# Optimization experiments

Measured on AMD Instinct MI355X. Metric: run time of the kernel, lower is better.

The kernel has to match this reference:

```python
import jax, jax.numpy as jnp
import numpy as np

KH, KW, PAD = 32, 32, 10  # kernel_size and padding from NeuralMem.__init__


def setup_inputs() -> dict:
    key = jax.random.key(0)
    k1, k2, k3, k4 = jax.random.split(key, 4)
    image = jax.random.normal(k1, (64, 64, 3), dtype=jnp.float32)
    mem = jax.random.normal(k2, (8192, 3072), dtype=jnp.float32)    # faiss IndexFlatL2 bank (keys)
    mem2 = jax.random.normal(k3, (8192, 3072), dtype=jnp.float32)   # faiss reconstruction bank (values)
    mapping = jax.random.randint(k4, (8192,), 0, 8192)              # Counter.most_common(1) vote table
    return {"image": image, "mem": mem, "mem2": mem2, "mapping": mapping}


def reference(image, mem, mem2, mapping):
    H, W, C = image.shape
    x = image.transpose(2, 0, 1)                       # [C,H,W]  (permute(2,0,1))
    xp = jnp.pad(x, ((0, 0), (PAD, PAD), (PAD, PAD)))  # unfold padding
    Lh = H + 2 * PAD - KH + 1
    Lw = W + 2 * PAD - KW + 1
    ii = jnp.arange(Lh)[:, None] + jnp.arange(KH)[None, :]  # [Lh,KH]
    jj = jnp.arange(Lw)[:, None] + jnp.arange(KW)[None, :]  # [Lw,KW]
    # unfold: patches [C,Lh,KH,Lw,KW] -> [L, C*KH*KW] with torch's (C,kh,kw) column order
    patches = xp[:, ii[:, :, None, None], jj[None, None, :, :]]
    patches = patches.transpose(1, 3, 0, 2, 4).reshape(Lh * Lw, C * KH * KW)  # [L,D]
    # L2 kNN (k=1): argmin ||p - m||^2 = argmin (||m||^2 - 2 p.m); ||p||^2 is constant per row
    mem_sq = jnp.sum(mem * mem, axis=1)                # [N]
    scores = patches @ mem.T                           # [L,N]
    nn = jnp.argmin(mem_sq[None, :] - 2.0 * scores, axis=1)  # [L]
    # counter majority vote -> mem2 reconstruct
    recon = mem2[mapping[nn]]                          # [L,D]
    # fold (sum of overlapping patches), then crop padding
    rp = recon.reshape(Lh, Lw, C, KH, KW).transpose(2, 0, 3, 1, 4)  # [C,Lh,KH,Lw,KW]
    outp = jnp.zeros_like(xp).at[:, ii[:, :, None, None], jj[None, None, :, :]].add(rp)
    out = outp[:, PAD:PAD + H, PAD:PAD + W]            # [C,H,W]
    out = out / jnp.max(out)                           # out / out.flatten().max()
    return out.transpose(1, 2, 0)                      # [H,W,C]
```

## Files before the change

kernel.cpp:

```cpp
#include <hip/hip_runtime.h>

typedef unsigned short u16;
typedef unsigned int   u32;
typedef unsigned long long u64;
typedef int      i32x4  __attribute__((ext_vector_type(4)));
typedef float    f32x4  __attribute__((ext_vector_type(4)));
typedef _Float16 f16x8  __attribute__((ext_vector_type(8)));

#define LHW   53
#define NP    2809
#define KDIM  3072
#define NMEM  8192
#define PADW  84
#define IMG   64
#define MPAD  2816
#define BIGF  3.402823466e+38f
#define MARGIN 24.0f
#define QS    31.75f
#define C2    (2.0f / (QS * QS))

#define O_XP    0UL
#define O_MSQ   84736UL
#define O_MI8   117504UL
#define O_AI8   25283328UL
#define O_D     33934080UL
#define O_PVAL  80071424UL
#define O_ROWI  81524480UL
#define O_ACC   81535744UL
#define WS_NEED5 81584896UL

#define F_XP    0
#define F_MSQ   21504
#define F_PVAL  29696
#define F_PIDX  119584
#define F_ROW   209472
#define F_ACC   212288
#define F_MAX   224576
#define NSPL    32
#define NRANGE  (NMEM / NSPL)

__device__ inline char q8(float x) {
    float y = x * QS;
    y = fminf(fmaxf(y, -127.f), 127.f);
    return (char)__float2int_rn(y);
}

__global__ void k_xp(const float* __restrict__ image, float* __restrict__ xp,
                     float* __restrict__ accb) {
    int id = blockIdx.x * 256 + threadIdx.x;
    if (id < 12288) accb[id] = 0.f;
    if (id < 3 * PADW * PADW) {
        int c = id / (PADW * PADW), rem = id % (PADW * PADW);
        int py = rem / PADW, px = rem % PADW;
        float v = 0.f;
        if (py >= 10 && py < 74 && px >= 10 && px < 74)
            v = image[((py - 10) * IMG + (px - 10)) * 3 + c];
        xp[id] = v;
    }
}

__global__ __launch_bounds__(1024) void k_maxnorm(const float* __restrict__ acc,
                                                  float* __restrict__ out) {
    int t = threadIdx.x;
    float m = -BIGF;
    for (int i = t; i < 12288; i += 1024) m = fmaxf(m, acc[i]);
    #pragma unroll
    for (int s = 1; s < 64; s <<= 1) m = fmaxf(m, __shfl_xor(m, s));
    __shared__ float ls[16];
    int lane = t & 63, w = t >> 6;
    if (lane == 0) ls[w] = m;
    __syncthreads();
    float mv = ls[0];
    #pragma unroll
    for (int i = 1; i < 16; ++i) mv = fmaxf(mv, ls[i]);
    for (int i = t; i < 12288; i += 1024) {
        int c = i >> 12, y = (i >> 6) & 63, x = i & 63;
        out[(y * IMG + x) * 3 + c] = acc[i] / mv;
    }
}

__global__ __launch_bounds__(256) void k_quantmsq(const float* __restrict__ mem,
                                                  char* __restrict__ mq,
                                                  float* __restrict__ msq) {
    int j = blockIdx.x, t = threadIdx.x;
    const float4* r4 = (const float4*)(mem + (size_t)j * KDIM);
    char4* q4 = (char4*)(mq + (size_t)j * KDIM);
    float s = 0.f;
    #pragma unroll
    for (int i = 0; i < 3; ++i) {
        int idx = i * 256 + t;
        float4 v = r4[idx];
        s += v.x * v.x + v.y * v.y + v.z * v.z + v.w * v.w;
        char4 q = {q8(v.x), q8(v.y), q8(v.z), q8(v.w)};
        q4[idx] = q;
    }
    #pragma unroll
    for (int m = 1; m < 64; m <<= 1) s += __shfl_xor(s, m);
    __shared__ float ls[4];
    int lane = t & 63, w = t >> 6;
    if (lane == 0) ls[w] = s;
    __syncthreads();
    if (t == 0) msq[j] = ls[0] + ls[1] + ls[2] + ls[3];
}

__global__ __launch_bounds__(256) void k_quant_A(const float* __restrict__ xp,
                                                 char* __restrict__ aq) {
    int id = blockIdx.x * 256 + threadIdx.x;
    int e0 = id * 4;
    int p = e0 / KDIM, k = e0 - p * KDIM;
    char4 q = {0, 0, 0, 0};
    if (p < NP) {
        int c = k >> 10, kh = (k >> 5) & 31, kw = k & 31;
        int lh = p / LHW, lw = p - lh * LHW;
        const float* src = xp + c * (PADW * PADW) + (lh + kh) * PADW + lw + kw;
        q.x = q8(src[0]); q.y = q8(src[1]); q.z = q8(src[2]); q.w = q8(src[3]);
    }
    ((char4*)aq)[id] = q;
}

__global__ __launch_bounds__(256) void k_gemm_i8(
    const char* __restrict__ Aq, const char* __restrict__ Bq,
    const float* __restrict__ msq, _Float16* __restrict__ Dm,
    float* __restrict__ pval)
{
    __shared__ __align__(16) char lds[65536];
    const int t = threadIdx.x;
    const int lane = t & 63;
    const int w = t >> 6, wm = w >> 1, wn = w & 1;
    const int mrow = lane & 15;

    int L = blockIdx.x;
    int logical = (L & 7) * 176 + (L >> 3);
    int by = logical / 22, bx = logical - by * 22;
    const int rowBase = bx * 128;
    const int jBase   = by * 128;

    const int lrow = lane >> 3;
    const int gsrc = (lane & 7) ^ lrow;
    const char* gpl[8];
    unsigned ldsb[8];
    #pragma unroll
    for (int s = 0; s < 8; ++s) {
        int P = s >> 2, sub = s & 3;
        int row = sub * 32 + w * 8 + lrow;
        const char* basep = (P == 0 ? Aq : Bq);
        int gRow = (P == 0 ? rowBase : jBase) + row;
        gpl[s]  = basep + (size_t)gRow * KDIM + gsrc * 16;
        ldsb[s] = P * 16384 + (unsigned)(sub * 32 + w * 8) * 128;
    }

    i32x4 acc[4][4];
    #pragma unroll
    for (int i = 0; i < 4; ++i)
        #pragma unroll
        for (int j = 0; j < 4; ++j) { i32x4 z = {0, 0, 0, 0}; acc[i][j] = z; }

    #pragma unroll
    for (int s = 0; s < 8; ++s)
        __builtin_amdgcn_global_load_lds(
            (const __attribute__((address_space(1))) void*)(gpl[s]),
            (__attribute__((address_space(3))) void*)(lds + ldsb[s]),
            16, 0, 0);

    for (int kc = 0; kc < 24; ++kc) {
        const int cb = kc & 1;
        __syncthreads();
        if (kc < 23) {
            const unsigned nb = (cb ^ 1) * 32768u;
            #pragma unroll
            for (int s = 0; s < 8; ++s)
                __builtin_amdgcn_global_load_lds(
                    (const __attribute__((address_space(1))) void*)(gpl[s] + (kc + 1) * 128),
                    (__attribute__((address_space(3))) void*)(lds + nb + ldsb[s]),
                    16, 0, 0);
        }
        const char* lbase = lds + cb * 32768;
        #pragma unroll
        for (int kh2 = 0; kh2 < 2; ++kh2) {
            const int grp = kh2 * 4 + (lane >> 4);
            i32x4 ah[4];
            #pragma unroll
            for (int f = 0; f < 4; ++f) {
                int ra = wm * 64 + f * 16 + mrow;
                ah[f] = *(const i32x4*)(lbase + ra * 128 + (grp ^ (ra & 7)) * 16);
            }
            #pragma unroll
            for (int fj = 0; fj < 4; ++fj) {
                int rb = wn * 64 + fj * 16 + mrow;
                i32x4 bh = *(const i32x4*)(lbase + 16384 + rb * 128 + (grp ^ (rb & 7)) * 16);
                #pragma unroll
                for (int fi = 0; fi < 4; ++fi)
                    acc[fi][fj] = __builtin_amdgcn_mfma_i32_16x16x64_i8(ah[fi], bh, acc[fi][fj], 0, 0, 0);
            }
        }
    }

    float ms[4];
    #pragma unroll
    for (int fj = 0; fj < 4; ++fj) ms[fj] = msq[jBase + wn * 64 + fj * 16 + mrow] - 3072.0f;
    const int splitId = by * 2 + wn;
    #pragma unroll
    for (int fi = 0; fi < 4; ++fi) {
        #pragma unroll
        for (int r = 0; r < 4; ++r) {
            int p = rowBase + wm * 64 + fi * 16 + (lane >> 4) * 4 + r;
            float bv = BIGF;
            #pragma unroll
            for (int fj = 0; fj < 4; ++fj) {
                int j = jBase + wn * 64 + fj * 16 + mrow;
                float d = fmaf(-C2, (float)acc[fi][fj][r], ms[fj]);
                Dm[(size_t)p * NMEM + j] = (_Float16)d;
                bv = fminf(bv, d);
            }
            #pragma unroll
            for (int m = 1; m < 16; m <<= 1) bv = fminf(bv, __shfl_xor(bv, m));
            if (mrow == 0 && p < NP)
                pval[(size_t)p * 128 + splitId] = bv;
        }
    }
}

__global__ __launch_bounds__(256) void k_refine(
    const _Float16* __restrict__ Dm, const float* __restrict__ pval,
    const float* __restrict__ msq, const float* __restrict__ xp,
    const float* __restrict__ mem, const int* __restrict__ mapping,
    int* __restrict__ rowIdx)
{
    const int p = blockIdx.x, t = threadIdx.x;
    const _Float16* row = Dm + (size_t)p * NMEM;
    const int lane = t & 63, w = t >> 6;

    __shared__ float wred[4];
    __shared__ int lcnt;
    __shared__ int list[256];
    __shared__ float thr_s;

    float pm = (t < 128) ? pval[(size_t)p * 128 + t] : BIGF;
    #pragma unroll
    for (int m = 1; m < 64; m <<= 1) pm = fminf(pm, __shfl_xor(pm, m));
    if (lane == 0) wred[w] = pm;
    if (t == 0) lcnt = 0;
    __syncthreads();
    if (t == 0)
        thr_s = fminf(fminf(wred[0], wred[1]), fminf(wred[2], wred[3]))
                + (MARGIN + 0.5f);
    __syncthreads();
    const float th = thr_s;

    #pragma unroll
    for (int i0 = 0; i0 < 4; ++i0) {
        int base = i0 * 2048 + t * 8;
        f16x8 v = *(const f16x8*)(row + base);
        #pragma unroll
        for (int e = 0; e < 8; ++e)
            if ((float)v[e] <= th) {
                int sl = atomicAdd(&lcnt, 1);
                if (sl < 256) list[sl] = base + e;
            }
    }
    __syncthreads();
    int nc = min(lcnt, 256);

    const int lh = p / LHW, lw = p - (p / LHW) * LHW;
    float bd = BIGF; int bj = 0x7fffffff;
    __shared__ float tot;
    for (int ci = 0; ci < nc; ++ci) {
        int j = list[ci];
        const float* mrow2 = mem + (size_t)j * KDIM;
        float s = 0.f;
        for (int k = t; k < KDIM; k += 256) {
            int c = k >> 10, kh = (k >> 5) & 31, kw = k & 31;
            s += xp[c * (PADW * PADW) + (lh + kh) * PADW + lw + kw] * mrow2[k];
        }
        #pragma unroll
        for (int m = 1; m < 64; m <<= 1) s += __shfl_xor(s, m);
        if (lane == 0) wred[w] = s;
        __syncthreads();
        if (t == 0) tot = wred[0] + wred[1] + wred[2] + wred[3];
        __syncthreads();
        float d = msq[j] - 2.f * tot;
        if (d < bd || (d == bd && j < bj)) { bd = d; bj = j; }
    }
    if (t == 0) rowIdx[p] = mapping[bj];
}

__global__ __launch_bounds__(256) void k_scatter(const float* __restrict__ mem2,
                                                 const int* __restrict__ rowIdx,
                                                 float* __restrict__ accb) {
    const int lh = blockIdx.x / 3, c = blockIdx.x % 3;
    __shared__ float accs[32 * 85];
    __shared__ int r2s[53];
    const int t = threadIdx.x;
    for (int i = t; i < 32 * 85; i += 256) accs[i] = 0.f;
    if (t < 53) r2s[t] = rowIdx[lh * LHW + t];
    __syncthreads();
    const int kh  = t >> 3;
    const int kwb = (t & 7) * 4;
    const size_t coff = (size_t)c * 1024 + kh * 32 + kwb;
    float* a0 = accs + kh * 85 + kwb;
    for (int lw = 0; lw < 53; ++lw) {
        const float4 v = *(const float4*)(mem2 + (size_t)r2s[lw] * KDIM + coff);
        float* a = a0 + lw;
        a[0] += v.x; a[1] += v.y; a[2] += v.z; a[3] += v.w;
        __syncthreads();
    }
    for (int i = t; i < 32 * 84; i += 256) {
        int kh2 = i / 84, px = i - kh2 * 84;
        int y = lh + kh2 - 10, x = px - 10;
        if (y >= 0 && y < 64 && x >= 0 && x < 64)
            atomicAdd(&accb[c * 4096 + y * 64 + x], accs[kh2 * 85 + px]);
    }
}

__global__ __launch_bounds__(256) void k_msq(const float* __restrict__ mem,
                                             float* __restrict__ msq) {
    int j = blockIdx.x;
    const float* row = mem + (size_t)j * KDIM;
    float s = 0.f;
    for (int i = threadIdx.x; i < KDIM; i += 256) { float v = row[i]; s += v * v; }
    #pragma unroll
    for (int m = 1; m < 64; m <<= 1) s += __shfl_xor(s, m);
    __shared__ float ls[4];
    int lane = threadIdx.x & 63, w = threadIdx.x >> 6;
    if (lane == 0) ls[w] = s;
    __syncthreads();
    if (threadIdx.x == 0) msq[j] = ls[0] + ls[1] + ls[2] + ls[3];
}

__global__ void k_amin(const float* __restrict__ pval, const int* __restrict__ pidx,
                       const int* __restrict__ mapping, int* __restrict__ rowIdx,
                       int nspl) {
    int p = blockIdx.x * 256 + threadIdx.x;
    if (p < NP) {
        float bv = BIGF; int bi = 0x7fffffff;
        for (int ns = 0; ns < nspl; ++ns) {
            float v = pval[(size_t)p * nspl + ns];
            int ix = pidx[(size_t)p * nspl + ns];
            if (v < bv || (v == bv && ix < bi)) { bv = v; bi = ix; }
        }
        rowIdx[p] = mapping[bi];
    }
}

__global__ __launch_bounds__(256) void k_gather(const float* __restrict__ mem2,
                                                const int* __restrict__ rowIdx,
                                                float* __restrict__ acc) {
    int b = blockIdx.x;
    int c = b >> 12, y = (b >> 6) & 63, x = b & 63;
    int khmin = max(0, y - 42), khmax = min(31, y + 10);
    int kwmin = max(0, x - 42), kwmax = min(31, x + 10);
    int nh = khmax - khmin + 1, nw = kwmax - kwmin + 1;
    int total = nh * nw;
    float s = 0.f;
    for (int idx = threadIdx.x; idx < total; idx += 256) {
        int kh = khmin + idx / nw;
        int kw = kwmin + idx % nw;
        int lh = y + 10 - kh, lw = x + 10 - kw;
        int p = lh * LHW + lw;
        int r2 = rowIdx[p];
        s += mem2[(size_t)r2 * KDIM + c * 1024 + kh * 32 + kw];
    }
    #pragma unroll
    for (int m = 1; m < 64; m <<= 1) s += __shfl_xor(s, m);
    __shared__ float ls[4];
    int lane = threadIdx.x & 63, w = threadIdx.x >> 6;
    if (lane == 0) ls[w] = s;
    __syncthreads();
    if (threadIdx.x == 0) acc[b] = ls[0] + ls[1] + ls[2] + ls[3];
}

__global__ __launch_bounds__(256) void k_gemm_argmin(
    const float* __restrict__ xp, const float* __restrict__ mem,
    const float* __restrict__ msq, float* __restrict__ pval,
    int* __restrict__ pidx)
{
    __shared__ float At[64][33];
    __shared__ float Bt[64][33];
    const int t = threadIdx.x;
    const int tx = t & 15, ty = t >> 4;
    const int rowBase = blockIdx.x * 64;
    const int nBase = blockIdx.y * NRANGE;

    float best[4]; int bidx[4];
    #pragma unroll
    for (int i = 0; i < 4; ++i) { best[i] = BIGF; bidx[i] = 0x7fffffff; }

    for (int nt = 0; nt < NRANGE / 64; ++nt) {
        const int jBase = nBase + nt * 64;
        float acc[4][4];
        #pragma unroll
        for (int i = 0; i < 4; ++i)
            #pragma unroll
            for (int j = 0; j < 4; ++j) acc[i][j] = 0.f;

        for (int kc = 0; kc < KDIM / 32; ++kc) {
            const int c = kc >> 5, kh = kc & 31;
            const float* xpc = xp + c * (PADW * PADW) + kh * PADW;
            #pragma unroll
            for (int i = 0; i < 8; ++i) {
                int e = i * 256 + t;
                int r = e >> 5, kwi = e & 31;
                int p = rowBase + r;
                float v = 0.f;
                if (p < NP) {
                    int lh = p / LHW, lw = p - lh * LHW;
                    v = xpc[lh * PADW + lw + kwi];
                }
                At[r][kwi] = v;
            }
            const float* mb = mem + (size_t)jBase * KDIM + kc * 32;
            #pragma unroll
            for (int i = 0; i < 8; ++i) {
                int e = i * 256 + t;
                int r = e >> 5, kwi = e & 31;
                Bt[r][kwi] = mb[(size_t)r * KDIM + kwi];
            }
            __syncthreads();
            #pragma unroll
            for (int kk = 0; kk < 32; ++kk) {
                float a[4], b[4];
                #pragma unroll
                for (int i = 0; i < 4; ++i) a[i] = At[ty + 16 * i][kk];
                #pragma unroll
                for (int j = 0; j < 4; ++j) b[j] = Bt[tx + 16 * j][kk];
                #pragma unroll
                for (int i = 0; i < 4; ++i)
                    #pragma unroll
                    for (int j = 0; j < 4; ++j) acc[i][j] += a[i] * b[j];
            }
            __syncthreads();
        }
        #pragma unroll
        for (int j = 0; j < 4; ++j) {
            int col = jBase + tx + 16 * j;
            float msv = msq[col];
            #pragma unroll
            for (int i = 0; i < 4; ++i) {
                float d = msv - 2.f * acc[i][j];
                if (d < best[i] || (d == best[i] && col < bidx[i])) {
                    best[i] = d; bidx[i] = col;
                }
            }
        }
    }
    #pragma unroll
    for (int m = 1; m < 16; m <<= 1) {
        #pragma unroll
        for (int i = 0; i < 4; ++i) {
            float ov = __shfl_xor(best[i], m);
            int   oi = __shfl_xor(bidx[i], m);
            if (ov < best[i] || (ov == best[i] && oi < bidx[i])) {
                best[i] = ov; bidx[i] = oi;
            }
        }
    }
    if (tx == 0) {
        #pragma unroll
        for (int i = 0; i < 4; ++i) {
            int p = rowBase + ty + 16 * i;
            if (p < NP) {
                pval[p * NSPL + blockIdx.y] = best[i];
                pidx[p * NSPL + blockIdx.y] = bidx[i];
            }
        }
    }
}

__global__ __launch_bounds__(256) void k_max(const float* __restrict__ acc,
                                             float* __restrict__ maxv) {
    float m = -BIGF;
    for (int i = threadIdx.x; i < 12288; i += 256) m = fmaxf(m, acc[i]);
    #pragma unroll
    for (int s = 1; s < 64; s <<= 1) m = fmaxf(m, __shfl_xor(m, s));
    __shared__ float ls[4];
    int lane = threadIdx.x & 63, w = threadIdx.x >> 6;
    if (lane == 0) ls[w] = m;
    __syncthreads();
    if (threadIdx.x == 0)
        maxv[0] = fmaxf(fmaxf(ls[0], ls[1]), fmaxf(ls[2], ls[3]));
}

__global__ void k_norm(const float* __restrict__ acc, const float* __restrict__ maxv,
                       float* __restrict__ out) {
    int id = blockIdx.x * 256 + threadIdx.x;
    if (id < 12288) {
        int c = id >> 12, y = (id >> 6) & 63, x = id & 63;
        out[(y * IMG + x) * 3 + c] = acc[id] / maxv[0];
    }
}

extern "C" void kernel_launch(void* const* d_in, const int* in_sizes, int n_in,
                              void* d_out, int out_size, void* d_ws, size_t ws_size,
                              hipStream_t stream) {
    const float* image   = (const float*)d_in[0];
    const float* mem     = (const float*)d_in[1];
    const float* mem2    = (const float*)d_in[2];
    const int*   mapping = (const int*)d_in[3];

    if (ws_size >= WS_NEED5) {
        char* wsB = (char*)d_ws;
        float*    xp   = (float*)(wsB + O_XP);
        float*    msq  = (float*)(wsB + O_MSQ);
        char*     mI8  = (char*)(wsB + O_MI8);
        char*     aI8  = (char*)(wsB + O_AI8);
        _Float16* Dm   = (_Float16*)(wsB + O_D);
        float*    pval = (float*)(wsB + O_PVAL);
        int*      rowI = (int*)(wsB + O_ROWI);
        float*    accb = (float*)(wsB + O_ACC);

        k_xp<<<dim3((3 * PADW * PADW + 255) / 256), 256, 0, stream>>>(image, xp, accb);
        k_quantmsq<<<dim3(NMEM), 256, 0, stream>>>(mem, mI8, msq);
        k_quant_A<<<dim3(MPAD * KDIM / 4 / 256), 256, 0, stream>>>(xp, aI8);
        k_gemm_i8<<<dim3(1408), 256, 0, stream>>>(aI8, mI8, msq, Dm, pval);
        k_refine<<<dim3(NP), 256, 0, stream>>>(Dm, pval, msq, xp, mem, mapping, rowI);
        k_scatter<<<dim3(LHW * 3), 256, 0, stream>>>(mem2, rowI, accb);
        k_maxnorm<<<dim3(1), 1024, 0, stream>>>(accb, (float*)d_out);
    } else {
        float* ws   = (float*)d_ws;
        float* xp   = ws + F_XP;
        float* msq  = ws + F_MSQ;
        float* pval = ws + F_PVAL;
        int*   pidx = (int*)(ws + F_PIDX);
        int*   rowI = (int*)(ws + F_ROW);
        float* acc  = ws + F_ACC;
        float* maxv = ws + F_MAX;

        k_xp<<<dim3((3 * PADW * PADW + 255) / 256), 256, 0, stream>>>(image, xp, acc);
        k_msq<<<dim3(NMEM), 256, 0, stream>>>(mem, msq);
        k_gemm_argmin<<<dim3((NP + 63) / 64, NSPL), 256, 0, stream>>>(xp, mem, msq, pval, pidx);
        k_amin<<<dim3((NP + 255) / 256), 256, 0, stream>>>(pval, pidx, mapping, rowI, NSPL);
        k_gather<<<dim3(3 * IMG * IMG), 256, 0, stream>>>(mem2, rowI, acc);
        k_max<<<dim3(1), 256, 0, stream>>>(acc, maxv);
        k_norm<<<dim3((12288 + 255) / 256), 256, 0, stream>>>(acc, maxv, (float*)d_out);
    }
}
```

Baseline: 199.0 us.

## Split fold scatter across lw chunks with register accumulators instead of shared memory

The fold/scatter kernel now launches four times as many blocks, each covering a chunk of 14 patch columns. Each thread keeps its output-column sums in registers, so the shared-memory accumulator and the per-iteration barrier are gone. This is meant to raise parallelism and remove the serialized lw loop with __syncthreads. In exchange there are more global atomicAdds into the output, the row loads are scalar and uncoalesced with per-element bounds checks, and skipping zero sums adds branching.

After: 202.2 us. No clear change (+1.6%).

```diff
diff --git a/kernel.cpp b/kernel.cpp
--- a/kernel.cpp
+++ b/kernel.cpp
@@ -2,7 +2,6 @@
 
 typedef unsigned short u16;
 typedef unsigned int   u32;
-typedef unsigned long long u64;
 typedef int      i32x4  __attribute__((ext_vector_type(4)));
 typedef float    f32x4  __attribute__((ext_vector_type(4)));
 typedef _Float16 f16x8  __attribute__((ext_vector_type(8)));
@@ -284,31 +283,40 @@
     if (t == 0) rowIdx[p] = mapping[bj];
 }
 
+#define LWCH 4
 __global__ __launch_bounds__(256) void k_scatter(const float* __restrict__ mem2,
                                                  const int* __restrict__ rowIdx,
                                                  float* __restrict__ accb) {
-    const int lh = blockIdx.x / 3, c = blockIdx.x % 3;
-    __shared__ float accs[32 * 85];
+    int b = blockIdx.x;
+    int ch = b & (LWCH - 1);
+    int lc = b >> 2;
+    const int lh = lc / 3, c = lc % 3;
+    const int lw0 = ch * 14, lw1 = min(53, lw0 + 14);
     __shared__ int r2s[53];
     const int t = threadIdx.x;
-    for (int i = t; i < 32 * 85; i += 256) accs[i] = 0.f;
-    if (t < 53) r2s[t] = rowIdx[lh * LHW + t];
-    __syncthreads();
-    const int kh  = t >> 3;
-    const int kwb = (t & 7) * 4;
-    const size_t coff = (size_t)c * 1024 + kh * 32 + kwb;
-    float* a0 = accs + kh * 85 + kwb;
-    for (int lw = 0; lw < 53; ++lw) {
-        const float4 v = *(const float4*)(mem2 + (size_t)r2s[lw] * KDIM + coff);
-        float* a = a0 + lw;
-        a[0] += v.x; a[1] += v.y; a[2] += v.z; a[3] += v.w;
-        __syncthreads();
-    }
-    for (int i = t; i < 32 * 84; i += 256) {
-        int kh2 = i / 84, px = i - kh2 * 84;
-        int y = lh + kh2 - 10, x = px - 10;
-        if (y >= 0 && y < 64 && x >= 0 && x < 64)
-            atomicAdd(&accb[c * 4096 + y * 64 + x], accs[kh2 * 85 + px]);
+    if (t >= lw0 && t < lw1) r2s[t] = rowIdx[lh * LHW + t];
+    __syncthreads();
+    const int kh = t >> 3;
+    const int g  = t & 7;
+    float s[11];
+    #pragma unroll
+    for (int u = 0; u < 11; ++u) s[u] = 0.f;
+    for (int lw = lw0; lw < lw1; ++lw) {
+        const float* rowp = mem2 + (size_t)r2s[lw] * KDIM + c * 1024 + kh * 32;
+        #pragma unroll
+        for (int u = 0; u < 11; ++u) {
+            int kw = g + 8 * u - lw;
+            if (kw >= 0 && kw < 32) s[u] += rowp[kw];
+        }
+    }
+    const int y = lh + kh - 10;
+    if (y >= 0 && y < 64) {
+        #pragma unroll
+        for (int u = 0; u < 11; ++u) {
+            int x = g + 8 * u - 10;
+            if (x >= 0 && x < 64 && s[u] != 0.f)
+                atomicAdd(&accb[c * 4096 + y * 64 + x], s[u]);
+        }
     }
 }
 
@@ -513,7 +521,7 @@
         k_quant_A<<<dim3(MPAD * KDIM / 4 / 256), 256, 0, stream>>>(xp, aI8);
         k_gemm_i8<<<dim3(1408), 256, 0, stream>>>(aI8, mI8, msq, Dm, pval);
         k_refine<<<dim3(NP), 256, 0, stream>>>(Dm, pval, msq, xp, mem, mapping, rowI);
-        k_scatter<<<dim3(LHW * 3), 256, 0, stream>>>(mem2, rowI, accb);
+        k_scatter<<<dim3(LHW * 3 * LWCH), 256, 0, stream>>>(mem2, rowI, accb);
         k_maxnorm<<<dim3(1), 1024, 0, stream>>>(accb, (float*)d_out);
     } else {
         float* ws   = (float*)d_ws;
```
